# Performance work log

Measured on AMD Instinct MI355X. Metric: run time of the kernel, lower is better.

## Reference

```python
import jax, jax.numpy as jnp
import numpy as np

B, C, H, W = 8, 256, 96, 96
NQ, NCLS = 100, 12
OBJ_CH = NCLS - 2 + 1  # 11
EPS = 1e-6


def conv2d(x, w, b, pad):
    out = jax.lax.conv_general_dilated(x, w, (1, 1), [(pad, pad), (pad, pad)],
                                       dimension_numbers=('NCHW', 'OIHW', 'NCHW'))
    return out + b[None, :, None, None]


def conv1d(x, w, b):
    out = jax.lax.conv_general_dilated(x, w, (1,), [(0, 0)],
                                       dimension_numbers=('NCH', 'OIH', 'NCH'))
    return out + b[None, :, None]


def adaptive_avg_pool_1d(x, out_size):
    # x: [..., L]; torch AdaptiveAvgPool semantics: bin i = mean(x[floor(i*L/o):ceil((i+1)*L/o)])
    L = x.shape[-1]
    i = np.arange(out_size)
    starts = (i * L) // out_size
    ends = -((-(i + 1) * L) // out_size)
    csum = jnp.concatenate([jnp.zeros(x.shape[:-1] + (1,), x.dtype), jnp.cumsum(x, -1)], -1)
    sizes = jnp.asarray((ends - starts).astype(np.float32))
    return (csum[..., ends] - csum[..., starts]) / sizes


def local_max(p):
    # 8-neighbor local maximum with zero padding, thresholded at EPS
    pd = jnp.pad(p, ((0, 0), (0, 0), (1, 1), (1, 1)))
    m = ((p >= pd[:, :, :-2, 1:-1]) & (p >= pd[:, :, 2:, 1:-1]) &
         (p >= pd[:, :, 1:-1, :-2]) & (p >= pd[:, :, 1:-1, 2:]) &
         (p >= pd[:, :, :-2, :-2]) & (p >= pd[:, :, :-2, 2:]) &
         (p >= pd[:, :, 2:, :-2]) & (p >= pd[:, :, 2:, 2:]) & (p >= EPS))
    return m.astype(p.dtype)


def mask_and_nms(probs):
    # one-hot mask from argmax over foreground channels, then add local-max map
    oh = jax.nn.one_hot(jnp.argmax(probs[:, :-1], axis=1), probs.shape[1], axis=1, dtype=probs.dtype)
    p = probs * oh
    return p + local_max(p)


def head(x, w1, b1, w2, b2):
    return conv2d(jax.nn.relu(conv2d(x, w1, b1, 1)), w2, b2, 0)


def setup_inputs() -> dict:
    key = jax.random.key(0)
    ks = jax.random.split(key, 20)
    rn = lambda k, s: jax.random.normal(k, s, jnp.float32) * 0.02
    z = lambda n: jnp.zeros((n,), jnp.float32)
    return {
        'x': jax.random.normal(ks[0], (B, C, H, W), jnp.float32),
        'y': jax.random.normal(ks[1], (B, C, H, W), jnp.float32),
        'pos_embeddings': jax.random.normal(ks[2], (1, C, H, W), jnp.float32),
        'lw1': rn(ks[3], (C, C, 3, 3)), 'lb1': z(C),
        'lw2': rn(ks[4], (2, C, 1, 1)), 'lb2': z(2),
        'rw1': rn(ks[5], (C, C, 3, 3)), 'rb1': z(C),
        'rw2': rn(ks[6], (2, C, 1, 1)), 'rb2': z(2),
        'ow1': rn(ks[7], (C, C, 3, 3)), 'ob1': z(C),
        'ow2': rn(ks[8], (OBJ_CH, C, 1, 1)), 'ob2': z(OBJ_CH),
        'cw1': rn(ks[9], (64, C, 3, 3)), 'cb1': z(64),
        'cw2': rn(ks[10], (32, 64, 3, 3)), 'cb2': z(32),
        'cm_lw': rn(ks[11], (778 * 2, 778 * 32)), 'cm_lb': z(778 * 2),
        'c1d_w': rn(ks[12], (C, 2, 3)), 'c1d_b': z(C),
        'q_lw': rn(ks[13], (NQ * C, C)), 'q_lb': z(NQ * C),
    }


def reference(x, y, pos_embeddings, lw1, lb1, lw2, lb2, rw1, rb1, rw2, rb2,
              ow1, ob1, ow2, ob2, cw1, cb1, cw2, cb2, cm_lw, cm_lb,
              c1d_w, c1d_b, q_lw, q_lb):
    b = x.shape[0]
    left_logits = head(x, lw1, lb1, lw2, lb2)
    right_logits = head(x, rw1, rb1, rw2, rb2)
    obj_logits = head(x, ow1, ob1, ow2, ob2)

    left_p = mask_and_nms(jax.nn.softmax(left_logits, axis=1))
    right_p = mask_and_nms(jax.nn.softmax(right_logits, axis=1))
    obj_p = mask_and_nms(jax.nn.softmax(obj_logits, axis=1))

    hw = H * W
    idx_l = jax.lax.top_k(left_p[:, 0].reshape(b, hw), 40)[1]
    idx_r = jax.lax.top_k(right_p[:, 0].reshape(b, hw), 40)[1]
    idx_o = jax.lax.top_k(obj_p[:, :-1].reshape(b, OBJ_CH - 1, hw).max(axis=1), 20)[1]
    idx = jnp.concatenate([idx_l, idx_r, idx_o], axis=1)  # [B, 100]

    xf = x.reshape(b, C, hw)
    topk_proposals = jnp.take_along_axis(xf, jnp.broadcast_to(idx[:, None, :], (b, C, NQ)), axis=2)
    pf = jnp.broadcast_to(pos_embeddings, (b, C, H, W)).reshape(b, C, hw)
    topk_pos = jnp.take_along_axis(pf, jnp.broadcast_to(idx[:, None, :], (b, C, NQ)), axis=2)

    # contact map estimation branch
    h = jax.nn.relu(conv2d(y, cw1, cb1, 1))
    h = jax.nn.relu(conv2d(h, cw2, cb2, 1))  # [B,32,H,W]
    h = jnp.mean(h, axis=3)                  # adaptive pool width -> 1
    h = adaptive_avg_pool_1d(h, 778)         # [B,32,778]
    cm = h.reshape(b, -1) @ cm_lw.T + cm_lb  # [B,1556]
    contact_map = cm.reshape(b, 2, 778, 1)

    # ContactMapConvolution
    cc = conv1d(contact_map.reshape(b, 2, 778), c1d_w, c1d_b)  # [B,C,776]
    cc = jnp.mean(cc, axis=2)                                  # [B,C]
    feat = (cc @ q_lw.T + q_lb).reshape(b, C, NQ)              # [B,C,100]

    topk_proposals = topk_proposals + feat
    return (topk_proposals, topk_pos, left_logits, right_logits, obj_logits, contact_map)
```

## Files before the change

### kernel.cpp

```cpp
#include <hip/hip_runtime.h>
#include <float.h>
#include <math.h>

#define B_ 8
#define C_ 256
#define H_ 96
#define W_ 96
#define HW_ 9216
#define NQ_ 100
#define EPS_ 1e-6f
#define PADW_ 98
#define PADIMG_ 9604
#define PALLOC_ 76880

typedef unsigned short ushort_t;
typedef __attribute__((ext_vector_type(8))) short bf16x8;
typedef __attribute__((ext_vector_type(16))) float f32x16;

typedef __attribute__((address_space(3))) unsigned int as3_u32;
typedef __attribute__((address_space(1))) unsigned int as1_u32;

__device__ __forceinline__ void gl16(const void* g, void* l) {
    __builtin_amdgcn_global_load_lds(
        (const as1_u32*)(unsigned long long)g,
        (as3_u32*)(unsigned int)(unsigned long long)l, 16, 0, 0);
}

__device__ __forceinline__ ushort_t bf16_of(float v) {
    unsigned u = __float_as_uint(v);
    u += 0x7fffu + ((u >> 16) & 1u);
    return (ushort_t)(u >> 16);
}
__device__ __forceinline__ float f_of_bf16(ushort_t h) {
    return __uint_as_float((unsigned)h << 16);
}

__global__ __launch_bounds__(256)
void zero_border_kernel(ushort_t* __restrict__ bh, ushort_t* __restrict__ bl, int Cch)
{
    int per = 388 * Cch / 8;
    int id = blockIdx.x * 256 + threadIdx.x;
    if (id >= 8 * per) return;
    int b = id / per, i = id - b * per;
    int pi = (i * 8) / Cch, c8 = (i * 8) % Cch;
    int yy, xx;
    if (pi < 98)      { yy = 0;            xx = pi; }
    else if (pi < 196){ yy = 97;           xx = pi - 98; }
    else if (pi < 292){ yy = pi - 195;     xx = 0; }
    else              { yy = pi - 291;     xx = 97; }
    size_t base = ((size_t)b * PADIMG_ + yy * PADW_ + xx) * Cch + c8;
    *(bf16x8*)&bh[base] = (bf16x8)(short)0;
    *(bf16x8*)&bl[base] = (bf16x8)(short)0;
}

__global__ __launch_bounds__(256)
void tsplit_kernel(const float* __restrict__ in, ushort_t* __restrict__ oh,
                   ushort_t* __restrict__ ol, int Cch)
{
    __shared__ float T[32][33];
    const int tx = threadIdx.x & 31, ty = threadIdx.x >> 5;
    const int p0 = blockIdx.x * 32, ci0 = blockIdx.y * 32, b = blockIdx.z;
#pragma unroll
    for (int i = 0; i < 4; ++i)
        T[ty + 8*i][tx] = in[((size_t)b*Cch + ci0 + ty + 8*i)*HW_ + p0 + tx];
    __syncthreads();
    const int y = p0 / 96, x0 = p0 - y * 96;
    const size_t Pp = (size_t)b*PADIMG_ + (size_t)(y + 1)*PADW_ + x0 + 1;
#pragma unroll
    for (int i = 0; i < 4; ++i) {
        float v = T[tx][ty + 8*i];
        ushort_t hi = bf16_of(v);
        float lo = v - f_of_bf16(hi);
        size_t o = (Pp + ty + 8*i)*Cch + ci0 + tx;
        oh[o] = hi;
        ol[o] = bf16_of(lo);
    }
}

__global__ __launch_bounds__(256)
void repack_kernel(const float* __restrict__ w, ushort_t* __restrict__ wh,
                   ushort_t* __restrict__ wl, int Cout, int Cin)
{
    int id = blockIdx.x*256 + threadIdx.x;
    int tot = 9*Cout*Cin;
    if (id >= tot) return;
    int tap = id / (Cout*Cin);
    int r   = id - tap*(Cout*Cin);
    int g   = r / (Cout*16);
    int r2  = r - g*(Cout*16);
    int oc  = r2 >> 4, cr = r2 & 15;
    int ci  = g*16 + cr;
    float v = w[((size_t)oc*Cin + ci)*9 + tap];
    ushort_t hi = bf16_of(v);
    wh[id] = hi;
    wl[id] = bf16_of(v - f_of_bf16(hi));
}

template<int WM, int WN, int MFR, int NFR, int CIN, int MODE, int KK>
__global__ __launch_bounds__(WM*WN*64, (WM*WN + 3) / 4)
void conv_gemm_kernel(const ushort_t* __restrict__ Agh, const ushort_t* __restrict__ Agl,
                      const ushort_t* __restrict__ Wgh, const ushort_t* __restrict__ Wgl,
                      const float* __restrict__ bias1,
                      const float* __restrict__ w2, const float* __restrict__ b2,
                      float* __restrict__ out_logits,
                      ushort_t* __restrict__ Oth, ushort_t* __restrict__ Otl,
                      float* __restrict__ outf)
{
    constexpr int NW    = WM*WN;
    constexpr int NT    = NW*64;
    constexpr int BM    = WM*MFR*32;
    constexpr int COUT  = WN*NFR*32;
    constexpr int NG    = CIN/16;
    constexpr int APAD  = 512;
    constexpr int ASZ   = 2*APAD*16;
    constexpr int AROUNDS = 32;
    static_assert(BM == 288, "BM must be 288");

    __shared__ __align__(16) ushort_t ALds[2*ASZ];

    const int tid  = threadIdx.x;
    const int lane = tid & 63;
    const int wid  = __builtin_amdgcn_readfirstlane(tid >> 6);
    const int wm   = wid / WN, wn = wid % WN;
    const int l31  = lane & 31, hh2 = lane >> 5;
    const int wnb  = wn * NFR * 32;

    const int cpx = gridDim.x >> 3;
    const int bid = (blockIdx.x & 7)*cpx + (blockIdx.x >> 3);
    const int bidx = bid >> 5;
    const int br   = bid & 31;
    const size_t S = (size_t)bidx*PADIMG_ + (size_t)(3*br)*PADW_;

    auto stageA = [&](int g, int sel) {
        ushort_t* dst = ALds + sel*ASZ;
#pragma unroll 1
        for (int c = wid; c < AROUNDS; c += NW) {
            int id = c*64 + lane;
            int split = id >> 10;
            int r2 = id & 1023;
            int row = r2 >> 1, slot = r2 & 1;
            int ch = slot ^ ((row >> 2) & 1);
            const ushort_t* src = (split ? Agl : Agh) + (S + row)*CIN + g*16 + ch*8;
            gl16(src, dst + (size_t)c*512);
        }
    };

    f32x16 acc[MFR][NFR];
#pragma unroll
    for (int i = 0; i < MFR; ++i)
#pragma unroll
        for (int j = 0; j < NFR; ++j)
#pragma unroll
            for (int r = 0; r < 16; ++r) acc[i][j][r] = 0.f;

    bf16x8 bh0[NFR], bl0[NFR], bh1[NFR], bl1[NFR], bh2[NFR], bl2[NFR];

#define LOADB(G, T, BH, BL)                                                    \
    {                                                                          \
        _Pragma("unroll")                                                      \
        for (int nf = 0; nf < NFR; ++nf) {                                     \
            size_t o = ((size_t)((T)*NG + (G))*COUT + (wnb + nf*32 + l31))*16  \
                       + hh2*8;                                                \
            BH[nf] = *(const bf16x8*)&Wgh[o];                                  \
            BL[nf] = *(const bf16x8*)&Wgl[o];                                  \
        }                                                                      \
    }

    stageA(0, 0);
    LOADB(0, 0, bh0, bl0);
    LOADB(0, 1, bh1, bl1);
    __builtin_amdgcn_sched_barrier(0);
    asm volatile("s_waitcnt vmcnt(%0)" :: "n"(4*NFR) : "memory");
    __builtin_amdgcn_s_barrier();
    __builtin_amdgcn_sched_barrier(0);

#define TAPBODY(T, BHC, BLC, BHN, BLN)                                         \
    {                                                                          \
        if ((T) <= 6)            LOADB(g,     (T)+2, BHN, BLN)                 \
        else if (g + 1 < NG)     LOADB(g+1,   (T)-7, BHN, BLN)                 \
        const int tapoff = ((T)/3)*PADW_ + ((T) % 3);                          \
        _Pragma("unroll")                                                      \
        for (int mf = 0; mf < MFR; ++mf) {                                     \
            int row = wm*PADW_ + tapoff + mf*32 + l31;                         \
            int o = abase + row*16 + ((hh2 ^ ((row >> 2) & 1)) << 3);          \
            bf16x8 ah = *(const bf16x8*)&ALds[o];                              \
            bf16x8 al = *(const bf16x8*)&ALds[o + APAD*16];                    \
            _Pragma("unroll")                                                  \
            for (int nf = 0; nf < NFR; ++nf) {                                 \
                acc[mf][nf] = __builtin_amdgcn_mfma_f32_32x32x16_bf16(         \
                    ah, BHC[nf], acc[mf][nf], 0, 0, 0);                        \
                acc[mf][nf] = __builtin_amdgcn_mfma_f32_32x32x16_bf16(         \
                    al, BHC[nf], acc[mf][nf], 0, 0, 0);                        \
                acc[mf][nf] = __builtin_amdgcn_mfma_f32_32x32x16_bf16(         \
                    ah, BLC[nf], acc[mf][nf], 0, 0, 0);                        \
            }                                                                  \
        }                                                                      \
    }

#pragma unroll 1
    for (int g = 0; g < NG; ++g) {
        if (g + 1 < NG) stageA(g + 1, (g + 1) & 1);
        const int abase = (g & 1) * ASZ;
        TAPBODY(0, bh0, bl0, bh2, bl2);
        TAPBODY(1, bh1, bl1, bh0, bl0);
        TAPBODY(2, bh2, bl2, bh1, bl1);
        TAPBODY(3, bh0, bl0, bh2, bl2);
        TAPBODY(4, bh1, bl1, bh0, bl0);
        TAPBODY(5, bh2, bl2, bh1, bl1);
        TAPBODY(6, bh0, bl0, bh2, bl2);
        TAPBODY(7, bh1, bl1, bh0, bl0);
        TAPBODY(8, bh2, bl2, bh1, bl1);
        __builtin_amdgcn_sched_barrier(0);
        asm volatile("s_waitcnt vmcnt(%0)" :: "n"(4*NFR) : "memory");
        __builtin_amdgcn_s_barrier();
        __builtin_amdgcn_sched_barrier(0);
    }
#undef TAPBODY
#undef LOADB
    __syncthreads();

    float biasv[NFR];
#pragma unroll
    for (int nf = 0; nf < NFR; ++nf) biasv[nf] = bias1[wnb + nf*32 + l31];

    if constexpr (MODE == 0) {
        float* Lacc = (float*)ALds;
        float w2v[NFR][KK];
#pragma unroll
        for (int nf = 0; nf < NFR; ++nf)
#pragma unroll
            for (int k = 0; k < KK; ++k)
                w2v[nf][k] = w2[(size_t)k*COUT + wnb + nf*32 + l31];

#pragma unroll
        for (int mf = 0; mf < MFR; ++mf) {
#pragma unroll
            for (int r = 0; r < 16; ++r) {
                float v[KK];
#pragma unroll
                for (int k = 0; k < KK; ++k) v[k] = 0.f;
#pragma unroll
                for (int nf = 0; nf < NFR; ++nf) {
                    float rr = fmaxf(acc[mf][nf][r] + biasv[nf], 0.f);
#pragma unroll
                    for (int k = 0; k < KK; ++k) v[k] += rr * w2v[nf][k];
                }
#pragma unroll
                for (int k = 0; k < KK; ++k) {
                    v[k] += __shfl_xor(v[k], 1);
                    v[k] += __shfl_xor(v[k], 2);
                    v[k] += __shfl_xor(v[k], 4);
                    v[k] += __shfl_xor(v[k], 8);
                    v[k] += __shfl_xor(v[k], 16);
                }
                if (l31 == 0) {
                    int crow = (r & 3) + 8*(r >> 2) + 4*hh2;
                    int mrow = wm*96 + mf*32 + crow;
#pragma unroll
                    for (int k = 0; k < KK; ++k)
                        Lacc[((size_t)wn*BM + mrow)*KK + k] = v[k];
                }
            }
        }
        __syncthreads();
        for (int i = tid; i < BM*KK; i += NT) {
            int mrow = i / KK, k = i - mrow*KK;
            float s = b2[k];
#pragma unroll
            for (int w = 0; w < WN; ++w) s += Lacc[((size_t)w*BM + mrow)*KK + k];
            out_logits[((size_t)bidx*KK + k)*HW_ + br*288 + mrow] = s;
        }
    } else if constexpr (MODE == 1) {
#pragma unroll
        for (int mf = 0; mf < MFR; ++mf)
#pragma unroll
            for (int nf = 0; nf < NFR; ++nf)
#pragma unroll
                for (int r = 0; r < 16; ++r) {
                    float rr = fmaxf(acc[mf][nf][r] + biasv[nf], 0.f);
                    ushort_t hi = bf16_of(rr);
                    float lo = rr - f_of_bf16(hi);
                    int crow = (r & 3) + 8*(r >> 2) + 4*hh2;
                    int xx = mf*32 + crow;
                    size_t Pp = (size_t)bidx*PADIMG_
                              + (size_t)(3*br + wm + 1)*PADW_ + xx + 1;
                    size_t o = Pp*COUT + wnb + nf*32 + l31;
                    Oth[o] = hi;
                    Otl[o] = bf16_of(lo);
                }
    } else {
        float (*T)[BM + 1] = (float(*)[BM + 1])ALds;
#pragma unroll
        for (int mf = 0; mf < MFR; ++mf)
#pragma unroll
            for (int r = 0; r < 16; ++r) {
                float rr = fmaxf(acc[mf][0][r] + biasv[0], 0.f);
                int crow = (r & 3) + 8*(r >> 2) + 4*hh2;
                T[l31][wm*96 + mf*32 + crow] = rr;
            }
        __syncthreads();
        for (int i = tid; i < COUT*BM; i += NT) {
            int c = i / BM, m = i - c*BM;
            outf[((size_t)bidx*COUT + c)*HW_ + br*288 + m] = T[c][m];
        }
    }
}

__global__ __launch_bounds__(256)
void prob2_kernel(const float* __restrict__ logits, float* __restrict__ p0)
{
    int i = blockIdx.x * 256 + threadIdx.x;
    if (i >= B_ * HW_) return;
    int b = i / HW_, pix = i - b * HW_;
    float l0 = logits[(size_t)b * 2 * HW_ + pix];
    float l1 = logits[(size_t)b * 2 * HW_ + HW_ + pix];
    float m = fmaxf(l0, l1);
    float e0 = expf(l0 - m), e1 = expf(l1 - m);
    p0[i] = e0 / (e0 + e1);
}

__global__ __launch_bounds__(256)
void score2_kernel(const float* __restrict__ p, float* __restrict__ sc)
{
    int i = blockIdx.x * 256 + threadIdx.x;
    if (i >= B_ * HW_) return;
    int pix = i % HW_;
    int yy = pix / W_, xx = pix - (pix / W_) * W_;
    float c = p[i];
    bool ok = (c >= EPS_);
    const float* pb = p + (i - pix);
#pragma unroll
    for (int dy = -1; dy <= 1; ++dy)
#pragma unroll
        for (int dx = -1; dx <= 1; ++dx) {
            if (dy == 0 && dx == 0) continue;
            int ny = yy + dy, nx = xx + dx;
            float v = 0.f;
            if (ny >= 0 && ny < H_ && nx >= 0 && nx < W_) v = pb[ny * W_ + nx];
            ok = ok && (c >= v);
        }
    sc[i] = c + (ok ? 1.f : 0.f);
}

__global__ __launch_bounds__(256)
void probobj_kernel(const float* __restrict__ logits, float* __restrict__ pval,
                    int* __restrict__ cstar)
{
    int i = blockIdx.x * 256 + threadIdx.x;
    if (i >= B_ * HW_) return;
    int b = i / HW_, pix = i - b * HW_;
    const float* lb = logits + (size_t)b * 11 * HW_ + pix;
    float l[11];
#pragma unroll
    for (int c2 = 0; c2 < 11; ++c2) l[c2] = lb[(size_t)c2 * HW_];
    float m = l[0];
#pragma unroll
    for (int c2 = 1; c2 < 11; ++c2) m = fmaxf(m, l[c2]);
    float sum = 0.f;
#pragma unroll
    for (int c2 = 0; c2 < 11; ++c2) sum += expf(l[c2] - m);
    int a = 0; float bestl = l[0];
#pragma unroll
    for (int c2 = 1; c2 < 10; ++c2)
        if (l[c2] > bestl) { bestl = l[c2]; a = c2; }
    pval[i] = expf(bestl - m) / sum;
    cstar[i] = a;
}

__global__ __launch_bounds__(256)
void score11_kernel(const float* __restrict__ p, const int* __restrict__ cs,
                    float* __restrict__ sc)
{
    int i = blockIdx.x * 256 + threadIdx.x;
    if (i >= B_ * HW_) return;
    int pix = i % HW_;
    int yy = pix / W_, xx = pix - (pix / W_) * W_;
    float c = p[i];
    int cc = cs[i];
    bool ok = (c >= EPS_);
    int base = i - pix;
#pragma unroll
    for (int dy = -1; dy <= 1; ++dy)
#pragma unroll
        for (int dx = -1; dx <= 1; ++dx) {
            if (dy == 0 && dx == 0) continue;
            int ny = yy + dy, nx = xx + dx;
            float v = 0.f;
            if (ny >= 0 && ny < H_ && nx >= 0 && nx < W_) {
                int n = base + ny * W_ + nx;
                v = (cs[n] == cc) ? p[n] : 0.f;
            }
            ok = ok && (c >= v);
        }
    sc[i] = c + (ok ? 1.f : 0.f);
}

__global__ __launch_bounds__(256)
void topk_kernel(const float* __restrict__ scL, const float* __restrict__ scR,
                 const float* __restrict__ scO, int* __restrict__ idx)
{
    __shared__ float sv[HW_];
    __shared__ float rv[256];
    __shared__ int   ri[256];
    const int h = blockIdx.x, b = blockIdx.y;
    const float* src = (h == 0) ? scL : (h == 1) ? scR : scO;
    const int k = (h == 2) ? 20 : 40;
// ... 106 lines not shown

__global__ __launch_bounds__(256)
void feat_kernel(const float* __restrict__ ccmean, const float* __restrict__ q_lw,
                 const float* __restrict__ q_lb, float* __restrict__ feat)
{
    __shared__ float cc[8][256];
    for (int t = threadIdx.x; t < 2048; t += 256) cc[t >> 8][t & 255] = ccmean[t];
    __syncthreads();
    int j = blockIdx.x * 256 + threadIdx.x;
    const float* wr = q_lw + (size_t)j * 256;
    float acc[8];
#pragma unroll
    for (int b = 0; b < 8; ++b) acc[b] = 0.f;
    for (int c = 0; c < 256; ++c) {
        float wv = wr[c];
#pragma unroll
        for (int b = 0; b < 8; ++b) acc[b] += wv * cc[b][c];
    }
    float qb = q_lb[j];
#pragma unroll
    for (int b = 0; b < 8; ++b) feat[(size_t)b * 25600 + j] = acc[b] + qb;
}

__global__ __launch_bounds__(256)
void gather_kernel(const float* __restrict__ x, const float* __restrict__ pos,
                   const float* __restrict__ feat, const int* __restrict__ idx,
                   float* __restrict__ out0, float* __restrict__ out1)
{
    int t = blockIdx.x * 256 + threadIdx.x;
    if (t >= B_ * C_ * NQ_) return;
    int q = t % NQ_;
    int c2 = (t / NQ_) % C_;
    int b = t / (C_ * NQ_);
    int p = idx[b * NQ_ + q];
    out0[t] = x[((size_t)b * C_ + c2) * HW_ + p] + feat[(size_t)b * 25600 + c2 * NQ_ + q];
    out1[t] = pos[(size_t)c2 * HW_ + p];
}

extern "C" void kernel_launch(void* const* d_in, const int* in_sizes, int n_in,
                              void* d_out, int out_size, void* d_ws, size_t ws_size,
                              hipStream_t stream) {
    const float* x    = (const float*)d_in[0];
    const float* y    = (const float*)d_in[1];
    const float* pos  = (const float*)d_in[2];
    const float* lw1  = (const float*)d_in[3];  const float* lb1 = (const float*)d_in[4];
    const float* lw2  = (const float*)d_in[5];  const float* lb2 = (const float*)d_in[6];
    const float* rw1  = (const float*)d_in[7];  const float* rb1 = (const float*)d_in[8];
    const float* rw2  = (const float*)d_in[9];  const float* rb2 = (const float*)d_in[10];
    const float* ow1  = (const float*)d_in[11]; const float* ob1 = (const float*)d_in[12];
    const float* ow2  = (const float*)d_in[13]; const float* ob2 = (const float*)d_in[14];
    const float* cw1  = (const float*)d_in[15]; const float* cb1 = (const float*)d_in[16];
    const float* cw2  = (const float*)d_in[17]; const float* cb2 = (const float*)d_in[18];
    const float* cmlw = (const float*)d_in[19]; const float* cmlb = (const float*)d_in[20];
    const float* c1dw = (const float*)d_in[21]; const float* c1db = (const float*)d_in[22];
    const float* qlw  = (const float*)d_in[23]; const float* qlb  = (const float*)d_in[24];

    float* out  = (float*)d_out;
    float* out0 = out;
    float* out1 = out + 204800;
    float* out2 = out + 409600;
    float* out3 = out + 557056;
    float* out4 = out + 704512;
    float* out5 = out + 1515520;

    float* ws = (float*)d_ws;
    ushort_t* Rh   = (ushort_t*)(ws);
    ushort_t* Rl   = (ushort_t*)(ws + 9840640);
    ushort_t* h1h  = (ushort_t*)(ws + 19681280);
    ushort_t* h1l  = (ushort_t*)(ws + 22141440);
    float*    h2   = ws + 24601600;
    ushort_t* wLh  = (ushort_t*)(ws + 26960896);
    ushort_t* wLl  = (ushort_t*)(ws + 27255808);
    ushort_t* wRh  = (ushort_t*)(ws + 27550720);
    ushort_t* wRl  = (ushort_t*)(ws + 27845632);
    ushort_t* wOh  = (ushort_t*)(ws + 28140544);
    ushort_t* wOl  = (ushort_t*)(ws + 28435456);
    ushort_t* wc1h = (ushort_t*)(ws + 28730368);
    ushort_t* wc1l = (ushort_t*)(ws + 28804096);
    ushort_t* wc2h = (ushort_t*)(ws + 28877824);
    ushort_t* wc2l = (ushort_t*)(ws + 28887040);
    float* pooled  = ws + 28896256;
    float* ccmean  = ws + 29095424;
    float* feat    = ws + 29097472;
    float* pmap    = ws + 29302272;
    int*   csmap   = (int*)(ws + 29376000);
    float* scL     = ws + 29449728;
    float* scR     = ws + 29523456;
    float* scO     = ws + 29597184;
    int*   idxb    = (int*)(ws + 29670912);
    (void)in_sizes; (void)n_in; (void)out_size; (void)ws_size; (void)pos;

    zero_border_kernel<<<388, 256, 0, stream>>>(Rh, Rl, 256);
    zero_border_kernel<<<97,  256, 0, stream>>>(h1h, h1l, 64);
    repack_kernel<<<(9*256*256+255)/256, 256, 0, stream>>>(lw1, wLh, wLl, 256, 256);
    repack_kernel<<<(9*256*256+255)/256, 256, 0, stream>>>(rw1, wRh, wRl, 256, 256);
    repack_kernel<<<(9*256*256+255)/256, 256, 0, stream>>>(ow1, wOh, wOl, 256, 256);
    repack_kernel<<<(9*64*256+255)/256,  256, 0, stream>>>(cw1, wc1h, wc1l, 64, 256);
    repack_kernel<<<(9*32*64+255)/256,   256, 0, stream>>>(cw2, wc2h, wc2l, 32, 64);

    tsplit_kernel<<<dim3(288, 8, 8), 256, 0, stream>>>(y, Rh, Rl, 256);
    conv_gemm_kernel<3,2,3,1,256,1,1><<<256, 384, 0, stream>>>(
        Rh, Rl, wc1h, wc1l, cb1, nullptr, nullptr, nullptr, h1h, h1l, nullptr);
    conv_gemm_kernel<3,1,3,1,64,2,1><<<256, 192, 0, stream>>>(
        h1h, h1l, wc2h, wc2l, cb2, nullptr, nullptr, nullptr, nullptr, nullptr, h2);
    pool_kernel<<<256, 128, 0, stream>>>(h2, pooled);
    cm_kernel<<<1556, 256, 0, stream>>>(pooled, cmlw, cmlb, out5);
    c1d_kernel<<<8, 256, 0, stream>>>(out5, c1dw, c1db, ccmean);
    feat_kernel<<<100, 256, 0, stream>>>(ccmean, qlw, qlb, feat);

    tsplit_kernel<<<dim3(288, 8, 8), 256, 0, stream>>>(x, Rh, Rl, 256);
    conv_gemm_kernel<3,4,3,2,256,0,2><<<256, 768, 0, stream>>>(
        Rh, Rl, wLh, wLl, lb1, lw2, lb2, out2, nullptr, nullptr, nullptr);
    conv_gemm_kernel<3,4,3,2,256,0,2><<<256, 768, 0, stream>>>(
        Rh, Rl, wRh, wRl, rb1, rw2, rb2, out3, nullptr, nullptr, nullptr);
    conv_gemm_kernel<3,4,3,2,256,0,11><<<256, 768, 0, stream>>>(
        Rh, Rl, wOh, wOl, ob1, ow2, ob2, out4, nullptr, nullptr, nullptr);

    prob2_kernel<<<288, 256, 0, stream>>>(out2, pmap);
    score2_kernel<<<288, 256, 0, stream>>>(pmap, scL);
    prob2_kernel<<<288, 256, 0, stream>>>(out3, pmap);
    score2_kernel<<<288, 256, 0, stream>>>(pmap, scR);
    probobj_kernel<<<288, 256, 0, stream>>>(out4, pmap, csmap);
    score11_kernel<<<288, 256, 0, stream>>>(pmap, csmap, scO);

    topk_kernel<<<dim3(3, 8), 256, 0, stream>>>(scL, scR, scO, idxb);
    gather_kernel<<<800, 256, 0, stream>>>(x, pos, feat, idxb, out0, out1);
}
```

Baseline: 1.182 ms.

## Split conv GEMM output channels across a second grid dimension with atomic logit reduction

Adds a blockIdx.y split over output channels so each conv GEMM block handles half (or a slice) of the output channels with fewer warps. This doubles the number of blocks over 256 CUs and raises the launch-bounds occupancy hint to 3. The 1x1 second-stage logits are now reduced with atomicAdd across channel slices, and a new kernel zeroes the three contiguous logit buffers beforehand; bias is added only by the first slice. In exchange, each block re-stages the same input tile, so A-operand traffic doubles, and atomics add contention and make the summation order nondeterministic.

```diff
diff --git a/kernel.cpp b/kernel.cpp
--- a/kernel.cpp
+++ b/kernel.cpp
@@ -15,6 +15,7 @@
 
 typedef unsigned short ushort_t;
 typedef __attribute__((ext_vector_type(8))) short bf16x8;
+typedef __attribute__((ext_vector_type(4))) float f32x4;
 typedef __attribute__((ext_vector_type(16))) float f32x16;
 
 typedef __attribute__((address_space(3))) unsigned int as3_u32;
@@ -54,6 +55,13 @@
 }
 
 __global__ __launch_bounds__(256)
+void zero_logits_kernel(float* __restrict__ p)
+{
+    int i = blockIdx.x * 256 + threadIdx.x;
+    if (i < 276480) ((f32x4*)p)[i] = (f32x4){0.f, 0.f, 0.f, 0.f};
+}
+
+__global__ __launch_bounds__(256)
 void tsplit_kernel(const float* __restrict__ in, ushort_t* __restrict__ oh,
                    ushort_t* __restrict__ ol, int Cch)
 {
@@ -96,8 +104,8 @@
     wl[id] = bf16_of(v - f_of_bf16(hi));
 }
 
-template<int WM, int WN, int MFR, int NFR, int CIN, int MODE, int KK>
-__global__ __launch_bounds__(WM*WN*64, (WM*WN + 3) / 4)
+template<int WM, int WN, int MFR, int NFR, int CIN, int MODE, int KK, int COT>
+__global__ __launch_bounds__(WM*WN*64, 3)
 void conv_gemm_kernel(const ushort_t* __restrict__ Agh, const ushort_t* __restrict__ Agl,
                       const ushort_t* __restrict__ Wgh, const ushort_t* __restrict__ Wgl,
                       const float* __restrict__ bias1,
@@ -123,6 +131,7 @@
     const int wid  = __builtin_amdgcn_readfirstlane(tid >> 6);
     const int wm   = wid / WN, wn = wid % WN;
     const int l31  = lane & 31, hh2 = lane >> 5;
+    const int ocbase = blockIdx.y * COUT;
     const int wnb  = wn * NFR * 32;
 
     const int cpx = gridDim.x >> 3;
@@ -159,8 +168,8 @@
     {                                                                          \
         _Pragma("unroll")                                                      \
         for (int nf = 0; nf < NFR; ++nf) {                                     \
-            size_t o = ((size_t)((T)*NG + (G))*COUT + (wnb + nf*32 + l31))*16  \
-                       + hh2*8;                                                \
+            size_t o = ((size_t)((T)*NG + (G))*COT                             \
+                        + (ocbase + wnb + nf*32 + l31))*16 + hh2*8;            \
             BH[nf] = *(const bf16x8*)&Wgh[o];                                  \
             BL[nf] = *(const bf16x8*)&Wgl[o];                                  \
         }                                                                      \
@@ -221,7 +230,7 @@
 
     float biasv[NFR];
 #pragma unroll
-    for (int nf = 0; nf < NFR; ++nf) biasv[nf] = bias1[wnb + nf*32 + l31];
+    for (int nf = 0; nf < NFR; ++nf) biasv[nf] = bias1[ocbase + wnb + nf*32 + l31];
 
     if constexpr (MODE == 0) {
         float* Lacc = (float*)ALds;
@@ -230,7 +239,7 @@
         for (int nf = 0; nf < NFR; ++nf)
 #pragma unroll
             for (int k = 0; k < KK; ++k)
-                w2v[nf][k] = w2[(size_t)k*COUT + wnb + nf*32 + l31];
+                w2v[nf][k] = w2[(size_t)k*COT + ocbase + wnb + nf*32 + l31];
 
 #pragma unroll
         for (int mf = 0; mf < MFR; ++mf) {
@@ -265,10 +274,10 @@
         __syncthreads();
         for (int i = tid; i < BM*KK; i += NT) {
             int mrow = i / KK, k = i - mrow*KK;
-            float s = b2[k];
+            float s = (blockIdx.y == 0) ? b2[k] : 0.f;
 #pragma unroll
             for (int w = 0; w < WN; ++w) s += Lacc[((size_t)w*BM + mrow)*KK + k];
-            out_logits[((size_t)bidx*KK + k)*HW_ + br*288 + mrow] = s;
+            atomicAdd(&out_logits[((size_t)bidx*KK + k)*HW_ + br*288 + mrow], s);
         }
     } else if constexpr (MODE == 1) {
 #pragma unroll
@@ -284,7 +293,7 @@
                     int xx = mf*32 + crow;
                     size_t Pp = (size_t)bidx*PADIMG_
                               + (size_t)(3*br + wm + 1)*PADW_ + xx + 1;
-                    size_t o = Pp*COUT + wnb + nf*32 + l31;
+                    size_t o = Pp*COT + ocbase + wnb + nf*32 + l31;
                     Oth[o] = hi;
                     Otl[o] = bf16_of(lo);
                 }
@@ -611,9 +620,9 @@
     repack_kernel<<<(9*32*64+255)/256,   256, 0, stream>>>(cw2, wc2h, wc2l, 32, 64);
 
     tsplit_kernel<<<dim3(288, 8, 8), 256, 0, stream>>>(y, Rh, Rl, 256);
-    conv_gemm_kernel<3,2,3,1,256,1,1><<<256, 384, 0, stream>>>(
+    conv_gemm_kernel<3,1,3,1,256,1,1,64><<<dim3(256,2), 192, 0, stream>>>(
         Rh, Rl, wc1h, wc1l, cb1, nullptr, nullptr, nullptr, h1h, h1l, nullptr);
-    conv_gemm_kernel<3,1,3,1,64,2,1><<<256, 192, 0, stream>>>(
+    conv_gemm_kernel<3,1,3,1,64,2,1,32><<<dim3(256,1), 192, 0, stream>>>(
         h1h, h1l, wc2h, wc2l, cb2, nullptr, nullptr, nullptr, nullptr, nullptr, h2);
     pool_kernel<<<256, 128, 0, stream>>>(h2, pooled);
     cm_kernel<<<1556, 256, 0, stream>>>(pooled, cmlw, cmlb, out5);
@@ -621,11 +630,12 @@
     feat_kernel<<<100, 256, 0, stream>>>(ccmean, qlw, qlb, feat);
 
     tsplit_kernel<<<dim3(288, 8, 8), 256, 0, stream>>>(x, Rh, Rl, 256);
-    conv_gemm_kernel<3,4,3,2,256,0,2><<<256, 768, 0, stream>>>(
+    zero_logits_kernel<<<1080, 256, 0, stream>>>(out2);
+    conv_gemm_kernel<3,2,3,2,256,0,2,256><<<dim3(256,2), 384, 0, stream>>>(
         Rh, Rl, wLh, wLl, lb1, lw2, lb2, out2, nullptr, nullptr, nullptr);
-    conv_gemm_kernel<3,4,3,2,256,0,2><<<256, 768, 0, stream>>>(
+    conv_gemm_kernel<3,2,3,2,256,0,2,256><<<dim3(256,2), 384, 0, stream>>>(
         Rh, Rl, wRh, wRl, rb1, rw2, rb2, out3, nullptr, nullptr, nullptr);
-    conv_gemm_kernel<3,4,3,2,256,0,11><<<256, 768, 0, stream>>>(
+    conv_gemm_kernel<3,2,3,2,256,0,11,256><<<dim3(256,2), 384, 0, stream>>>(
         Rh, Rl, wOh, wOl, ob1, ow2, ob2, out4, nullptr, nullptr, nullptr);
 
     prob2_kernel<<<288, 256, 0, stream>>>(out2, pmap);
```

Result: slower. 1.509 ms (+27.7%).

## Add small-block single-row conv kernel for right and object heads

Applied to the files above, without the earlier changes.

Adds a new conv_sb_kernel that computes one 96-pixel image row per block with 4 waves covering all 256 output channels. It uses a 768-block grid of 256 threads with a launch bound allowing 3 blocks per CU, instead of 256 large 768-thread blocks. The row of A is staged into LDS per 16-channel group, while B fragments are double-buffered in registers straight from global memory. The fused 1x1 second conv is reduced via cross-lane shuffles. The right and object heads now use it, while the left head keeps the old kernel, likely as an A/B comparison. The goal is better occupancy and load balance, at the cost of less reuse of A across rows and more weight traffic from global memory.

```diff
diff --git a/kernel.cpp b/kernel.cpp
--- a/kernel.cpp
+++ b/kernel.cpp
@@ -303,6 +303,185 @@
             int c = i / BM, m = i - c*BM;
             outf[((size_t)bidx*COUT + c)*HW_ + br*288 + m] = T[c][m];
         }
+    }
+}
+
+template<int MFR, int WN, int NFR, int CIN, int KK>
+__global__ __launch_bounds__(WN*64, 3)
+void conv_sb_kernel(const ushort_t* __restrict__ Agh, const ushort_t* __restrict__ Agl,
+                    const ushort_t* __restrict__ Wgh, const ushort_t* __restrict__ Wgl,
+                    const float* __restrict__ bias1,
+                    const float* __restrict__ w2, const float* __restrict__ b2,
+                    float* __restrict__ out_logits)
+{
+    constexpr int NW   = WN;
+    constexpr int NT   = NW*64;
+    constexpr int COUT = WN*NFR*32;
+    constexpr int NG   = CIN/16;
+    constexpr int APAD = 304;
+    constexpr int ASZ  = 2*APAD*16;
+    constexpr int AGR  = (4*APAD)/64;
+    static_assert(NG % 2 == 0, "");
+    static_assert(MFR == 3, "BM must be 96");
+
+    __shared__ __align__(16) ushort_t ALds[ASZ];
+
+    const int tid  = threadIdx.x;
+    const int lane = tid & 63;
+    const int wid  = __builtin_amdgcn_readfirstlane(tid >> 6);
+    const int wn   = wid;
+    const int l31  = lane & 31, hh2 = lane >> 5;
+    const int wnb  = wn * NFR * 32;
+
+    const int cpx = gridDim.x >> 3;
+    const int bid = (blockIdx.x & 7)*cpx + (blockIdx.x >> 3);
+    const int bidx = bid / 96;
+    const int prow = bid - bidx*96;
+    const int pimg0 = prow * 96;
+    const size_t S = (size_t)bidx*PADIMG_ + (size_t)prow*PADW_;
+
+    auto stageA = [&](int g) {
+#pragma unroll 1
+        for (int c = wid; c < AGR; c += NW) {
+            int id = c*64 + lane;
+            int split = id / (2*APAD);
+            int r2 = id % (2*APAD);
+            int row = r2 >> 1, slot = r2 & 1;
+            int ch = slot ^ ((row >> 2) & 1);
+            const ushort_t* src = (split ? Agl : Agh) + (S + row)*CIN + g*16 + ch*8;
+            gl16(src, ALds + (size_t)c*512);
+        }
+    };
+
+    f32x16 acc[MFR][NFR];
+#pragma unroll
+    for (int i = 0; i < MFR; ++i)
+#pragma unroll
+        for (int j = 0; j < NFR; ++j)
+#pragma unroll
+            for (int r = 0; r < 16; ++r) acc[i][j][r] = 0.f;
+
+    bf16x8 bhX[NFR], blX[NFR], bhY[NFR], blY[NFR];
+
+#define LOADB(G, T, BH, BL)                                                    \
+    {                                                                          \
+        _Pragma("unroll")                                                      \
+        for (int nf = 0; nf < NFR; ++nf) {                                     \
+            size_t o = ((size_t)((T)*NG + (G))*COUT + (wnb + nf*32 + l31))*16  \
+                       + hh2*8;                                                \
+            BH[nf] = *(const bf16x8*)&Wgh[o];                                  \
+            BL[nf] = *(const bf16x8*)&Wgl[o];                                  \
+        }                                                                      \
+    }
+
+#define TAPBODY(G, T, BHC, BLC, BHN, BLN)                                      \
+    {                                                                          \
+        if ((T) < 8)             LOADB((G), (T)+1, BHN, BLN)                   \
+        else if ((G) + 1 < NG)   LOADB((G)+1, 0, BHN, BLN)                     \
+        const int tapoff = ((T)/3)*PADW_ + ((T) % 3);                          \
+        _Pragma("unroll")                                                      \
+        for (int mf = 0; mf < MFR; ++mf) {                                     \
+            int row = tapoff + mf*32 + l31;                                    \
+            int o = row*16 + ((hh2 ^ ((row >> 2) & 1)) << 3);                  \
+            bf16x8 ah = *(const bf16x8*)&ALds[o];                              \
+            bf16x8 al = *(const bf16x8*)&ALds[o + APAD*16];                    \
+            _Pragma("unroll")                                                  \
+            for (int nf = 0; nf < NFR; ++nf) {                                 \
+                acc[mf][nf] = __builtin_amdgcn_mfma_f32_32x32x16_bf16(         \
+                    ah, BHC[nf], acc[mf][nf], 0, 0, 0);                        \
+                acc[mf][nf] = __builtin_amdgcn_mfma_f32_32x32x16_bf16(         \
+                    al, BHC[nf], acc[mf][nf], 0, 0, 0);                        \
+                acc[mf][nf] = __builtin_amdgcn_mfma_f32_32x32x16_bf16(         \
+                    ah, BLC[nf], acc[mf][nf], 0, 0, 0);                        \
+            }                                                                  \
+        }                                                                      \
+    }
+
+#define GROUPBODY(G, S0h, S0l, S1h, S1l)                                       \
+    {                                                                          \
+        TAPBODY((G), 0, S0h, S0l, S1h, S1l);                                   \
+        TAPBODY((G), 1, S1h, S1l, S0h, S0l);                                   \
+        TAPBODY((G), 2, S0h, S0l, S1h, S1l);                                   \
+        TAPBODY((G), 3, S1h, S1l, S0h, S0l);                                   \
+        TAPBODY((G), 4, S0h, S0l, S1h, S1l);                                   \
+        TAPBODY((G), 5, S1h, S1l, S0h, S0l);                                   \
+        TAPBODY((G), 6, S0h, S0l, S1h, S1l);                                   \
+        TAPBODY((G), 7, S1h, S1l, S0h, S0l);                                   \
+        TAPBODY((G), 8, S0h, S0l, S1h, S1l);                                   \
+    }
+
+#define STAGEWAIT(G)                                                           \
+    __builtin_amdgcn_s_barrier();            \
+    stageA(G);                                                                 \
+    __builtin_amdgcn_sched_barrier(0);                                         \
+    asm volatile("s_waitcnt vmcnt(0)" ::: "memory");                           \
+    __builtin_amdgcn_s_barrier();                                              \
+    __builtin_amdgcn_sched_barrier(0);
+
+    LOADB(0, 0, bhX, blX);
+
+#pragma unroll 1
+    for (int g = 0; g < NG; g += 2) {
+        STAGEWAIT(g)
+        GROUPBODY(g,     bhX, blX, bhY, blY);
+        STAGEWAIT(g + 1)
+        GROUPBODY(g + 1, bhY, blY, bhX, blX);
+    }
+#undef STAGEWAIT
+#undef GROUPBODY
+#undef TAPBODY
+#undef LOADB
+    __syncthreads();
+
+    float biasv[NFR];
+#pragma unroll
+    for (int nf = 0; nf < NFR; ++nf) biasv[nf] = bias1[wnb + nf*32 + l31];
+
+    float* Lacc = (float*)ALds;
+    float w2v[NFR][KK];
+#pragma unroll
+    for (int nf = 0; nf < NFR; ++nf)
+#pragma unroll
+        for (int k = 0; k < KK; ++k)
+            w2v[nf][k] = w2[(size_t)k*COUT + wnb + nf*32 + l31];
+
+#pragma unroll
+    for (int mf = 0; mf < MFR; ++mf) {
+#pragma unroll
+        for (int r = 0; r < 16; ++r) {
+            float v[KK];
+#pragma unroll
+            for (int k = 0; k < KK; ++k) v[k] = 0.f;
+#pragma unroll
+            for (int nf = 0; nf < NFR; ++nf) {
+                float rr = fmaxf(acc[mf][nf][r] + biasv[nf], 0.f);
+#pragma unroll
+                for (int k = 0; k < KK; ++k) v[k] += rr * w2v[nf][k];
+            }
+#pragma unroll
+            for (int k = 0; k < KK; ++k) {
+                v[k] += __shfl_xor(v[k], 1);
+                v[k] += __shfl_xor(v[k], 2);
+                v[k] += __shfl_xor(v[k], 4);
+                v[k] += __shfl_xor(v[k], 8);
+                v[k] += __shfl_xor(v[k], 16);
+            }
+            if (l31 == 0) {
+                int crow = (r & 3) + 8*(r >> 2) + 4*hh2;
+                int row96 = mf*32 + crow;
+#pragma unroll
+                for (int k = 0; k < KK; ++k)
+                    Lacc[((size_t)wn*96 + row96)*KK + k] = v[k];
+            }
+        }
+    }
+    __syncthreads();
+    for (int i = tid; i < 96*KK; i += NT) {
+        int row96 = i / KK, k = i - row96*KK;
+        float s = b2[k];
+#pragma unroll
+        for (int w = 0; w < WN; ++w) s += Lacc[((size_t)w*96 + row96)*KK + k];
+        out_logits[((size_t)bidx*KK + k)*HW_ + pimg0 + row96] = s;
     }
 }
 
@@ -623,10 +802,10 @@
     tsplit_kernel<<<dim3(288, 8, 8), 256, 0, stream>>>(x, Rh, Rl, 256);
     conv_gemm_kernel<3,4,3,2,256,0,2><<<256, 768, 0, stream>>>(
         Rh, Rl, wLh, wLl, lb1, lw2, lb2, out2, nullptr, nullptr, nullptr);
-    conv_gemm_kernel<3,4,3,2,256,0,2><<<256, 768, 0, stream>>>(
-        Rh, Rl, wRh, wRl, rb1, rw2, rb2, out3, nullptr, nullptr, nullptr);
-    conv_gemm_kernel<3,4,3,2,256,0,11><<<256, 768, 0, stream>>>(
-        Rh, Rl, wOh, wOl, ob1, ow2, ob2, out4, nullptr, nullptr, nullptr);
+    conv_sb_kernel<3,4,2,256,2><<<768, 256, 0, stream>>>(
+        Rh, Rl, wRh, wRl, rb1, rw2, rb2, out3);
+    conv_sb_kernel<3,4,2,256,11><<<768, 256, 0, stream>>>(
+        Rh, Rl, wOh, wOl, ob1, ow2, ob2, out4);
 
     prob2_kernel<<<288, 256, 0, stream>>>(out2, pmap);
     score2_kernel<<<288, 256, 0, stream>>>(pmap, scL);
```

Result: no change. 1.162 ms (-1.6%).

## Merge three head convs into one small-block kernel with atomic logit reduction

Applied to the files above, without the earlier changes.

Replaces the three separate 256-block head conv launches with a single 4608-block kernel. Each block computes one image row for a 128-output-channel slice of one head. The partial 1x1-conv logits are reduced across channel slices with atomicAdd into a pre-zeroed logits buffer. Per-head biases and second-layer weights are packed into shared arrays, and the left/right prob/score kernels are batched via blockIdx.y. The goal is better occupancy and load balance across CUs, at the cost of restaging A per block, float atomics that are nondeterministic in order, and an extra zeroing pass.

```diff
diff --git a/kernel.cpp b/kernel.cpp
--- a/kernel.cpp
+++ b/kernel.cpp
@@ -15,6 +15,7 @@
 
 typedef unsigned short ushort_t;
 typedef __attribute__((ext_vector_type(8))) short bf16x8;
+typedef __attribute__((ext_vector_type(4))) float f32x4;
 typedef __attribute__((ext_vector_type(16))) float f32x16;
 
 typedef __attribute__((address_space(3))) unsigned int as3_u32;
@@ -54,6 +55,13 @@
 }
 
 __global__ __launch_bounds__(256)
+void zero_logits_kernel(float* __restrict__ p)
+{
+    int i = blockIdx.x * 256 + threadIdx.x;
+    if (i < 276480) ((f32x4*)p)[i] = (f32x4){0.f, 0.f, 0.f, 0.f};
+}
+
+__global__ __launch_bounds__(256)
 void tsplit_kernel(const float* __restrict__ in, ushort_t* __restrict__ oh,
                    ushort_t* __restrict__ ol, int Cch)
 {
@@ -96,13 +104,37 @@
     wl[id] = bf16_of(v - f_of_bf16(hi));
 }
 
-template<int WM, int WN, int MFR, int NFR, int CIN, int MODE, int KK>
+__global__ __launch_bounds__(256)
+void pack_heads3_kernel(const float* lb1, const float* rb1, const float* ob1,
+                        const float* lw2, const float* rw2, const float* ow2,
+                        const float* lb2, const float* rb2, const float* ob2,
+                        float* __restrict__ bias1all, float* __restrict__ w2all,
+                        float* __restrict__ b2all)
+{
+    int i = blockIdx.x * 256 + threadIdx.x;
+    if (i < 768) bias1all[i] = (i < 256) ? lb1[i] : (i < 512) ? rb1[i-256] : ob1[i-512];
+    if (i < 33) {
+        int h = i / 11, k = i - h*11;
+        b2all[i] = (h == 0) ? (k < 2 ? lb2[k] : 0.f)
+                 : (h == 1) ? (k < 2 ? rb2[k] : 0.f)
+                 : ob2[k];
+    }
+    if (i < 3*11*256) {
+        int h = i / 2816, r = i - h*2816;
+        int k = r / 256, oc = r - k*256;
+        float v = 0.f;
+        if (h == 0)      { if (k < 2) v = lw2[k*256 + oc]; }
+        else if (h == 1) { if (k < 2) v = rw2[k*256 + oc]; }
+        else             v = ow2[k*256 + oc];
+        w2all[i] = v;
+    }
+}
+
+template<int WM, int WN, int MFR, int NFR, int CIN, int MODE>
 __global__ __launch_bounds__(WM*WN*64, (WM*WN + 3) / 4)
 void conv_gemm_kernel(const ushort_t* __restrict__ Agh, const ushort_t* __restrict__ Agl,
                       const ushort_t* __restrict__ Wgh, const ushort_t* __restrict__ Wgl,
                       const float* __restrict__ bias1,
-                      const float* __restrict__ w2, const float* __restrict__ b2,
-                      float* __restrict__ out_logits,
                       ushort_t* __restrict__ Oth, ushort_t* __restrict__ Otl,
                       float* __restrict__ outf)
 {
@@ -223,54 +255,7 @@
 #pragma unroll
     for (int nf = 0; nf < NFR; ++nf) biasv[nf] = bias1[wnb + nf*32 + l31];
 
-    if constexpr (MODE == 0) {
-        float* Lacc = (float*)ALds;
-        float w2v[NFR][KK];
-#pragma unroll
-        for (int nf = 0; nf < NFR; ++nf)
-#pragma unroll
-            for (int k = 0; k < KK; ++k)
-                w2v[nf][k] = w2[(size_t)k*COUT + wnb + nf*32 + l31];
-
-#pragma unroll
-        for (int mf = 0; mf < MFR; ++mf) {
-#pragma unroll
-            for (int r = 0; r < 16; ++r) {
-                float v[KK];
-#pragma unroll
-                for (int k = 0; k < KK; ++k) v[k] = 0.f;
-#pragma unroll
-                for (int nf = 0; nf < NFR; ++nf) {
-                    float rr = fmaxf(acc[mf][nf][r] + biasv[nf], 0.f);
-#pragma unroll
-                    for (int k = 0; k < KK; ++k) v[k] += rr * w2v[nf][k];
-                }
-#pragma unroll
-                for (int k = 0; k < KK; ++k) {
-                    v[k] += __shfl_xor(v[k], 1);
-                    v[k] += __shfl_xor(v[k], 2);
-                    v[k] += __shfl_xor(v[k], 4);
-                    v[k] += __shfl_xor(v[k], 8);
-                    v[k] += __shfl_xor(v[k], 16);
-                }
-                if (l31 == 0) {
-                    int crow = (r & 3) + 8*(r >> 2) + 4*hh2;
-                    int mrow = wm*96 + mf*32 + crow;
-#pragma unroll
-                    for (int k = 0; k < KK; ++k)
-                        Lacc[((size_t)wn*BM + mrow)*KK + k] = v[k];
-                }
-            }
-        }
-        __syncthreads();
-        for (int i = tid; i < BM*KK; i += NT) {
-            int mrow = i / KK, k = i - mrow*KK;
-            float s = b2[k];
-#pragma unroll
-            for (int w = 0; w < WN; ++w) s += Lacc[((size_t)w*BM + mrow)*KK + k];
-            out_logits[((size_t)bidx*KK + k)*HW_ + br*288 + mrow] = s;
-        }
-    } else if constexpr (MODE == 1) {
+    if constexpr (MODE == 1) {
 #pragma unroll
         for (int mf = 0; mf < MFR; ++mf)
 #pragma unroll
@@ -306,9 +291,174 @@
     }
 }
 
-__global__ __launch_bounds__(256)
-void prob2_kernel(const float* __restrict__ logits, float* __restrict__ p0)
-{
+__global__ __launch_bounds__(256, 4)
+void conv_sb3_kernel(const ushort_t* __restrict__ Agh, const ushort_t* __restrict__ Agl,
+                     const ushort_t* __restrict__ wLh, const ushort_t* __restrict__ wLl,
+                     const ushort_t* __restrict__ wRh, const ushort_t* __restrict__ wRl,
+                     const ushort_t* __restrict__ wOh, const ushort_t* __restrict__ wOl,
+                     const float* __restrict__ bias1all, const float* __restrict__ w2all,
+                     const float* __restrict__ b2all, float* __restrict__ out_logits)
+{
+    constexpr int NG = 16, APAD = 304, ASZ = 2*APAD*16, AGR = 19, MFR = 3;
+    __shared__ __align__(16) ushort_t ALds[ASZ];
+
+    const int tid  = threadIdx.x;
+    const int lane = tid & 63;
+    const int wid  = __builtin_amdgcn_readfirstlane(tid >> 6);
+    const int l31  = lane & 31, hh2 = lane >> 5;
+
+    const int cpx = gridDim.x >> 3;
+    const int bid = (blockIdx.x & 7)*cpx + (blockIdx.x >> 3);
+    const int h    = bid / 1536;
+    const int rr_  = bid - h*1536;
+    const int ocb  = rr_ / 768;
+    const int sub  = rr_ - ocb*768;
+    const int bidx = sub / 96, prow = sub - bidx*96;
+    const int pimg0 = prow * 96;
+    const size_t S = (size_t)bidx*PADIMG_ + (size_t)prow*PADW_;
+
+    const ushort_t* Wh = (h == 0) ? wLh : (h == 1) ? wRh : wOh;
+    const ushort_t* Wl = (h == 0) ? wLl : (h == 1) ? wRl : wOl;
+    const int oc0 = ocb*128 + wid*32;
+    const float* bias1 = bias1all + h*256;
+    const float* w2    = w2all + (size_t)h*2816;
+    const float* b2    = b2all + h*11;
+    const int kklim = (h == 2) ? 11 : 2;
+    float* dst = out_logits + ((h == 0) ? 0 : (h == 1) ? 147456 : 294912);
+
+    auto stageA = [&](int g) {
+#pragma unroll 1
+        for (int c = wid; c < AGR; c += 4) {
+            int id = c*64 + lane;
+            int split = id / (2*APAD);
+            int r2 = id % (2*APAD);
+            int row = r2 >> 1, slot = r2 & 1;
+            int ch = slot ^ ((row >> 2) & 1);
+            const ushort_t* src = (split ? Agl : Agh) + (S + row)*C_ + g*16 + ch*8;
+            gl16(src, ALds + (size_t)c*512);
+        }
+    };
+
+    f32x16 acc[MFR];
+#pragma unroll
+    for (int i = 0; i < MFR; ++i)
+#pragma unroll
+        for (int r = 0; r < 16; ++r) acc[i][r] = 0.f;
+
+    bf16x8 bhX, blX, bhY, blY;
+
+#define LOADB(G, T, BH, BL)                                                    \
+    {                                                                          \
+        size_t o = ((size_t)((T)*NG + (G))*256 + (oc0 + l31))*16 + hh2*8;      \
+        BH = *(const bf16x8*)&Wh[o];                                           \
+        BL = *(const bf16x8*)&Wl[o];                                           \
+    }
+
+#define TAPBODY(G, T, BHC, BLC, BHN, BLN)                                      \
+    {                                                                          \
+        if ((T) < 8)             LOADB((G), (T)+1, BHN, BLN)                   \
+        else if ((G) + 1 < NG)   LOADB((G)+1, 0, BHN, BLN)                     \
+        const int tapoff = ((T)/3)*PADW_ + ((T) % 3);                          \
+        _Pragma("unroll")                                                      \
+        for (int mf = 0; mf < MFR; ++mf) {                                     \
+            int row = tapoff + mf*32 + l31;                                    \
+            int o = row*16 + ((hh2 ^ ((row >> 2) & 1)) << 3);                  \
+            bf16x8 ah = *(const bf16x8*)&ALds[o];                              \
+            bf16x8 al = *(const bf16x8*)&ALds[o + APAD*16];                    \
+            acc[mf] = __builtin_amdgcn_mfma_f32_32x32x16_bf16(                 \
+                ah, BHC, acc[mf], 0, 0, 0);                                    \
+            acc[mf] = __builtin_amdgcn_mfma_f32_32x32x16_bf16(                 \
+                al, BHC, acc[mf], 0, 0, 0);                                    \
+            acc[mf] = __builtin_amdgcn_mfma_f32_32x32x16_bf16(                 \
+                ah, BLC, acc[mf], 0, 0, 0);                                    \
+        }                                                                      \
+    }
+
+#define GROUPBODY(G, S0h, S0l, S1h, S1l)                                       \
+    {                                                                          \
+        TAPBODY((G), 0, S0h, S0l, S1h, S1l);                                   \
+        TAPBODY((G), 1, S1h, S1l, S0h, S0l);                                   \
+        TAPBODY((G), 2, S0h, S0l, S1h, S1l);                                   \
+        TAPBODY((G), 3, S1h, S1l, S0h, S0l);                                   \
+        TAPBODY((G), 4, S0h, S0l, S1h, S1l);                                   \
+        TAPBODY((G), 5, S1h, S1l, S0h, S0l);                                   \
+        TAPBODY((G), 6, S0h, S0l, S1h, S1l);                                   \
+        TAPBODY((G), 7, S1h, S1l, S0h, S0l);                                   \
+        TAPBODY((G), 8, S0h, S0l, S1h, S1l);                                   \
+    }
+
+#define STAGEWAIT(G)                                                           \
+    __builtin_amdgcn_s_barrier();                                              \
+    stageA(G);                                                                 \
+    __builtin_amdgcn_sched_barrier(0);                                         \
+    asm volatile("s_waitcnt vmcnt(0)" ::: "memory");                           \
+    __builtin_amdgcn_s_barrier();                                              \
+    __builtin_amdgcn_sched_barrier(0);
+
+    LOADB(0, 0, bhX, blX);
+
+#pragma unroll 1
+    for (int g = 0; g < NG; g += 2) {
+        STAGEWAIT(g)
+        GROUPBODY(g,     bhX, blX, bhY, blY);
+        STAGEWAIT(g + 1)
+        GROUPBODY(g + 1, bhY, blY, bhX, blX);
+    }
+#undef STAGEWAIT
+#undef GROUPBODY
+#undef TAPBODY
+#undef LOADB
+    __syncthreads();
+
+    float biasv = bias1[oc0 + l31];
+    float w2v[11];
+#pragma unroll
+    for (int k = 0; k < 11; ++k) w2v[k] = w2[k*256 + oc0 + l31];
+
+    float* Lacc = (float*)ALds;
+#pragma unroll
+    for (int mf = 0; mf < MFR; ++mf) {
+#pragma unroll
+        for (int r = 0; r < 16; ++r) {
+            float rr2 = fmaxf(acc[mf][r] + biasv, 0.f);
+            float v[11];
+#pragma unroll
+            for (int k = 0; k < 11; ++k) {
+                if (k < kklim) {
+                    v[k] = rr2 * w2v[k];
+                    v[k] += __shfl_xor(v[k], 1);
+                    v[k] += __shfl_xor(v[k], 2);
+                    v[k] += __shfl_xor(v[k], 4);
+                    v[k] += __shfl_xor(v[k], 8);
+                    v[k] += __shfl_xor(v[k], 16);
+                } else v[k] = 0.f;
+            }
+            if (l31 == 0) {
+                int crow = (r & 3) + 8*(r >> 2) + 4*hh2;
+                int row96 = mf*32 + crow;
+#pragma unroll
+                for (int k = 0; k < 11; ++k)
+                    if (k < kklim)
+                        Lacc[((size_t)wid*96 + row96)*11 + k] = v[k];
+            }
+        }
+    }
+    __syncthreads();
+    for (int i = tid; i < 96*kklim; i += 256) {
+        int row96 = i / kklim, k = i - row96*kklim;
+        float s = (ocb == 0) ? b2[k] : 0.f;
+#pragma unroll
+        for (int w = 0; w < 4; ++w) s += Lacc[((size_t)w*96 + row96)*11 + k];
+        atomicAdd(&dst[((size_t)bidx*kklim + k)*HW_ + pimg0 + row96], s);
+    }
+}
+
+__global__ __launch_bounds__(256)
+void prob2b_kernel(const float* __restrict__ l2, const float* __restrict__ l3,
+                   float* __restrict__ pL, float* __restrict__ pR)
+{
+    const float* logits = blockIdx.y ? l3 : l2;
+    float* p0 = blockIdx.y ? pR : pL;
     int i = blockIdx.x * 256 + threadIdx.x;
     if (i >= B_ * HW_) return;
     int b = i / HW_, pix = i - b * HW_;
@@ -320,8 +470,11 @@
 }
 
 __global__ __launch_bounds__(256)
-void score2_kernel(const float* __restrict__ p, float* __restrict__ sc)
-{
+void score2b_kernel(const float* __restrict__ pL, const float* __restrict__ pR,
+                    float* __restrict__ sL, float* __restrict__ sR)
+{
+    const float* p = blockIdx.y ? pR : pL;
+    float* sc = blockIdx.y ? sR : sL;
     int i = blockIdx.x * 256 + threadIdx.x;
     if (i >= B_ * HW_) return;
     int pix = i % HW_;
@@ -594,12 +747,17 @@
     float* pooled  = ws + 28896256;
     float* ccmean  = ws + 29095424;
     float* feat    = ws + 29097472;
-    float* pmap    = ws + 29302272;
+    float* pmapL   = ws + 29302272;
     int*   csmap   = (int*)(ws + 29376000);
     float* scL     = ws + 29449728;
     float* scR     = ws + 29523456;
     float* scO     = ws + 29597184;
     int*   idxb    = (int*)(ws + 29670912);
+    float* bias1all= ws + 29671712;
+    float* w2all   = ws + 29672480;
+    float* b2all   = ws + 29680928;
+    float* pmapR   = ws + 29680976;
+    float* pmapO   = ws + 29754704;
     (void)in_sizes; (void)n_in; (void)out_size; (void)ws_size; (void)pos;
 
     zero_border_kernel<<<388, 256, 0, stream>>>(Rh, Rl, 256);
@@ -609,31 +767,28 @@
     repack_kernel<<<(9*256*256+255)/256, 256, 0, stream>>>(ow1, wOh, wOl, 256, 256);
     repack_kernel<<<(9*64*256+255)/256,  256, 0, stream>>>(cw1, wc1h, wc1l, 64, 256);
     repack_kernel<<<(9*32*64+255)/256,   256, 0, stream>>>(cw2, wc2h, wc2l, 32, 64);
+    pack_heads3_kernel<<<33, 256, 0, stream>>>(lb1, rb1, ob1, lw2, rw2, ow2,
+                                               lb2, rb2, ob2, bias1all, w2all, b2all);
 
     tsplit_kernel<<<dim3(288, 8, 8), 256, 0, stream>>>(y, Rh, Rl, 256);
-    conv_gemm_kernel<3,2,3,1,256,1,1><<<256, 384, 0, stream>>>(
-        Rh, Rl, wc1h, wc1l, cb1, nullptr, nullptr, nullptr, h1h, h1l, nullptr);
-    conv_gemm_kernel<3,1,3,1,64,2,1><<<256, 192, 0, stream>>>(
-        h1h, h1l, wc2h, wc2l, cb2, nullptr, nullptr, nullptr, nullptr, nullptr, h2);
+    conv_gemm_kernel<3,2,3,1,256,1><<<256, 384, 0, stream>>>(
+        Rh, Rl, wc1h, wc1l, cb1, h1h, h1l, nullptr);
+    conv_gemm_kernel<3,1,3,1,64,2><<<256, 192, 0, stream>>>(
+        h1h, h1l, wc2h, wc2l, cb2, nullptr, nullptr, h2);
     pool_kernel<<<256, 128, 0, stream>>>(h2, pooled);
     cm_kernel<<<1556, 256, 0, stream>>>(pooled, cmlw, cmlb, out5);
     c1d_kernel<<<8, 256, 0, stream>>>(out5, c1dw, c1db, ccmean);
     feat_kernel<<<100, 256, 0, stream>>>(ccmean, qlw, qlb, feat);
 
     tsplit_kernel<<<dim3(288, 8, 8), 256, 0, stream>>>(x, Rh, Rl, 256);
-    conv_gemm_kernel<3,4,3,2,256,0,2><<<256, 768, 0, stream>>>(
-        Rh, Rl, wLh, wLl, lb1, lw2, lb2, out2, nullptr, nullptr, nullptr);
-    conv_gemm_kernel<3,4,3,2,256,0,2><<<256, 768, 0, stream>>>(
-        Rh, Rl, wRh, wRl, rb1, rw2, rb2, out3, nullptr, nullptr, nullptr);
-    conv_gemm_kernel<3,4,3,2,256,0,11><<<256, 768, 0, stream>>>(
-        Rh, Rl, wOh, wOl, ob1, ow2, ob2, out4, nullptr, nullptr, nullptr);
-
-    prob2_kernel<<<288, 256, 0, stream>>>(out2, pmap);
-    score2_kernel<<<288, 256, 0, stream>>>(pmap, scL);
-    prob2_kernel<<<288, 256, 0, stream>>>(out3, pmap);
-    score2_kernel<<<288, 256, 0, stream>>>(pmap, scR);
-    probobj_kernel<<<288, 256, 0, stream>>>(out4, pmap, csmap);
-    score11_kernel<<<288, 256, 0, stream>>>(pmap, csmap, scO);
+    zero_logits_kernel<<<1080, 256, 0, stream>>>(out2);
+    conv_sb3_kernel<<<4608, 256, 0, stream>>>(
+        Rh, Rl, wLh, wLl, wRh, wRl, wOh, wOl, bias1all, w2all, b2all, out2);
+
+    prob2b_kernel<<<dim3(288, 2), 256, 0, stream>>>(out2, out3, pmapL, pmapR);
+    score2b_kernel<<<dim3(288, 2), 256, 0, stream>>>(pmapL, pmapR, scL, scR);
+    probobj_kernel<<<288, 256, 0, stream>>>(out4, pmapO, csmap);
+    score11_kernel<<<288, 256, 0, stream>>>(pmapO, csmap, scO);
 
     topk_kernel<<<dim3(3, 8), 256, 0, stream>>>(scL, scR, scO, idxb);
     gather_kernel<<<800, 256, 0, stream>>>(x, pos, feat, idxb, out0, out1);
```

New measurement: 1.470 ms. +24.4%, slower.
